# Performance work log

Hardware: AMD Instinct MI355X
Metric: run time of the kernel (lower is better)

Reference implementation:

```python
import jax, jax.numpy as jnp
import numpy as np

N_NODES = 100000
N_EDGES = 6400000
F_IN, F_HID, F_OUT = 5, 5, 10


def setup_inputs() -> dict:
    key = jax.random.key(0)
    ks = jax.random.split(key, 9)
    x = jax.random.normal(ks[0], (N_NODES, F_IN), dtype=jnp.float32)
    src = jax.random.randint(ks[1], (N_EDGES,), 0, N_NODES, dtype=jnp.int32)
    dst = jax.random.randint(ks[2], (N_EDGES,), 0, N_NODES, dtype=jnp.int32)
    s1 = 1.0 / np.sqrt(F_IN)
    s2 = 1.0 / np.sqrt(F_HID)
    W_self1 = jax.random.uniform(ks[3], (F_IN, F_HID), jnp.float32, -s1, s1)
    W_neigh1 = jax.random.uniform(ks[4], (F_IN, F_HID), jnp.float32, -s1, s1)
    b1 = jnp.zeros((F_HID,), jnp.float32)
    W_self2 = jax.random.uniform(ks[5], (F_HID, F_OUT), jnp.float32, -s2, s2)
    W_neigh2 = jax.random.uniform(ks[6], (F_HID, F_OUT), jnp.float32, -s2, s2)
    b2 = jnp.zeros((F_OUT,), jnp.float32)
    return {"x": x, "src": src, "dst": dst,
            "W_self1": W_self1, "W_neigh1": W_neigh1, "b1": b1,
            "W_self2": W_self2, "W_neigh2": W_neigh2, "b2": b2}


def _sage_mean(h, src, dst, W_self, W_neigh, b):
    # DGL SAGEConv (mean): out = h @ W_self + mean_{u->v}(h_u) @ W_neigh + b
    msg = h[src]                                        # [E, F] gather
    agg = jax.ops.segment_sum(msg, dst, num_segments=N_NODES)   # [N, F]
    deg = jax.ops.segment_sum(jnp.ones((src.shape[0],), h.dtype), dst,
                              num_segments=N_NODES)     # [N]
    h_neigh = agg / jnp.maximum(deg, 1.0)[:, None]
    return h @ W_self + h_neigh @ W_neigh + b


def reference(x, src, dst, W_self1, W_neigh1, b1, W_self2, W_neigh2, b2):
    h = jax.nn.sigmoid(_sage_mean(x, src, dst, W_self1, W_neigh1, b1))
    out = jax.nn.sigmoid(_sage_mean(h, src, dst, W_self2, W_neigh2, b2))
    return out
```

## Files before the change

### kernel.cpp

```cpp
#include <hip/hip_runtime.h>
#include <hip/hip_fp16.h>
#include <math.h>


#define F_IN  5
#define F_HID 5
#define F_OUT 10

#define NBSHIFT 7
#define NPB     (1 << NBSHIFT)
#define PBLK    1024
#define CHUNK   8192
#define EPT     8
#define BSTRIDE 9216
#define SBLK    512
#define SPT     18
#define LPN2    8
#define LBLK    256

__device__ __forceinline__ float sigmoidf(float v) {
    return 1.0f / (1.0f + __expf(-v));
}

__device__ __forceinline__ uint4 pack_h5(const float* __restrict__ xr) {
    float4 a = *(const float4*)xr;
    float a4 = xr[4];
    uint4 o;
    o.x = (unsigned)__half_as_ushort(__float2half_rn(a.x)) |
          ((unsigned)__half_as_ushort(__float2half_rn(a.y)) << 16);
    o.y = (unsigned)__half_as_ushort(__float2half_rn(a.z)) |
          ((unsigned)__half_as_ushort(__float2half_rn(a.w)) << 16);
    o.z = (unsigned)__half_as_ushort(__float2half_rn(a4));
    o.w = 0;
    return o;
}

__device__ __forceinline__ void acc5(uint4 q, float& a0, float& a1, float& a2,
                                     float& a3, float& a4) {
    float2 f01 = __half22float2(*(const __half2*)&q.x);
    float2 f23 = __half22float2(*(const __half2*)&q.y);
    float2 f45 = __half22float2(*(const __half2*)&q.z);
    a0 += f01.x; a1 += f01.y; a2 += f23.x; a3 += f23.y; a4 += f45.x;
}

__global__ void partition(const float* __restrict__ x,
                          const int* __restrict__ src, const int* __restrict__ dst,
                          int* __restrict__ bcursor, int* __restrict__ packed,
                          uint4* __restrict__ xh, int E, int N, int NB) {
    __shared__ int cnt[PBLK], excl[PBLK], adj[PBLK];
    __shared__ int wsum[16];
    __shared__ int buf[CHUNK];
    __shared__ unsigned char dlow[CHUNK];
    int t = threadIdx.x;
    int lane = t & 63, w = t >> 6;
    if (t < NPB) {
        int v = (blockIdx.x << NBSHIFT) + t;
        if (v < N) xh[v] = pack_h5(x + (size_t)v * 5);
    }
    cnt[t] = 0;
    __syncthreads();
    int base = blockIdx.x * CHUNK;
    int end  = min(base + CHUNK, E);
    int sarr[EPT], darr[EPT];
    #pragma unroll
    for (int r = 0; r < 2; ++r) {
        int i = base + r * 4096 + t * 4;
        if (i + 4 <= end) {
            int4 sv = *(const int4*)(src + i);
            int4 dv = *(const int4*)(dst + i);
            sarr[r*4+0]=sv.x; sarr[r*4+1]=sv.y; sarr[r*4+2]=sv.z; sarr[r*4+3]=sv.w;
            darr[r*4+0]=dv.x; darr[r*4+1]=dv.y; darr[r*4+2]=dv.z; darr[r*4+3]=dv.w;
        } else {
            #pragma unroll
            for (int c = 0; c < 4; ++c) {
                int i2 = i + c;
                if (i2 < end) { sarr[r*4+c] = src[i2]; darr[r*4+c] = dst[i2]; }
            }
        }
    }
    int esd[EPT];
    int ebp[EPT];
    #pragma unroll
    for (int j = 0; j < EPT; ++j) {
        int i = base + (j >> 2) * 4096 + t * 4 + (j & 3);
        if (i < end) {
            int sv = sarr[j], d = darr[j];
            int b  = d >> NBSHIFT;
            int p  = atomicAdd(&cnt[b], 1);
            esd[j] = sv | ((d & (NPB - 1)) << 17);
            ebp[j] = (b << 14) | p;
        }
    }
    __syncthreads();
    int v = cnt[t];
    int incl = v;
    #pragma unroll
    for (int off = 1; off < 64; off <<= 1) {
        int u = __shfl_up(incl, off, 64);
        if (lane >= off) incl += u;
    }
    if (lane == 63) wsum[w] = incl;
    __syncthreads();
    if (t < 16) {
        int s = wsum[t];
        #pragma unroll
        for (int off = 1; off < 16; off <<= 1) {
            int u = __shfl_up(s, off, 16);
            if (t >= off) s += u;
        }
        wsum[t] = s;
    }
    __syncthreads();
    int wbase = (w > 0) ? wsum[w - 1] : 0;
    excl[t] = incl - v + wbase;
    __syncthreads();
    if (t < NB) {
        int cb = cnt[t];
        int go = cb ? atomicAdd(&bcursor[t], cb) : 0;
        adj[t] = t * BSTRIDE + go - excl[t];
    }
    __syncthreads();
    #pragma unroll
    for (int j = 0; j < EPT; ++j) {
        int i = base + (j >> 2) * 4096 + t * 4 + (j & 3);
        if (i < end) {
            int b   = ebp[j] >> 14;
            int pos = excl[b] + (ebp[j] & 0x3FFF);
            buf[pos]  = (esd[j] & 0x1FFFF) | (b << 17);
            dlow[pos] = (unsigned char)(esd[j] >> 17);
        }
    }
    __syncthreads();
    int cval = end - base;
    for (int p = t; p < cval; p += PBLK) {
        int e = buf[p];
        int b = e >> 17;
        packed[adj[b] + p] = (e & 0x1FFFF) | ((int)dlow[p] << 17);
    }
}

__global__ void __launch_bounds__(SBLK, 8)
sortagg1(const uint4* __restrict__ xh, int* __restrict__ packed,
         const int* __restrict__ bcursor,
         const float* __restrict__ Ws, const float* __restrict__ Wn,
         const float* __restrict__ bias,
         uint4* __restrict__ hp, int2* __restrict__ sd, int N) {
    __shared__ int buf[BSTRIDE];
    __shared__ int ncnt[NPB], nst[NPB];
    __shared__ int w0sum;
    int b = blockIdx.x, t = threadIdx.x;
    int s0  = b * BSTRIDE;
    int cnt = min(bcursor[b], BSTRIDE);
    if (t < NPB) ncnt[t] = 0;
    __syncthreads();
    int myv[SPT];
    #pragma unroll
    for (int r = 0; r < 4; ++r) {
        int i = r * 2048 + t * 4;
        if (i + 4 <= cnt) {
            int4 q = *(const int4*)(packed + s0 + i);
            myv[r*4+0]=q.x; myv[r*4+1]=q.y; myv[r*4+2]=q.z; myv[r*4+3]=q.w;
        } else {
            #pragma unroll
            for (int c = 0; c < 4; ++c) {
                int i2 = i + c;
                myv[r*4+c] = (i2 < cnt) ? packed[s0 + i2] : 0;
            }
        }
    }
    {
        int i = 8192 + t * 2;
        if (i + 2 <= cnt) {
            int2 q = *(const int2*)(packed + s0 + i);
            myv[16] = q.x; myv[17] = q.y;
        } else {
            myv[16] = (i     < cnt) ? packed[s0 + i]     : 0;
            myv[17] = (i + 1 < cnt) ? packed[s0 + i + 1] : 0;
        }
    }
    short myp[SPT];
    #pragma unroll
    for (int j = 0; j < SPT; ++j) {
        int i = (j < 16) ? ((j >> 2) * 2048 + t * 4 + (j & 3)) : (8192 + t * 2 + (j - 16));
        if (i < cnt) {
            myp[j] = (short)atomicAdd(&ncnt[(myv[j] >> 17) & (NPB - 1)], 1);
        }
    }
    __syncthreads();
    if (t < NPB) {
        int lane = t & 63;
        int vv = ncnt[t];
        int incl = vv;
        #pragma unroll
        for (int off = 1; off < 64; off <<= 1) {
            int u = __shfl_up(incl, off, 64);
            if (lane >= off) incl += u;
        }
        if (t == 63) w0sum = incl;
        nst[t] = incl - vv;
    }
    __syncthreads();
    if (t >= 64 && t < NPB) nst[t] += w0sum;
    __syncthreads();
    if (t < NPB) {
        int node = (b << NBSHIFT) + t;
        if (node < N) sd[node] = make_int2(s0 + nst[t], ncnt[t]);
    }
    __syncthreads();
    #pragma unroll
    for (int j = 0; j < SPT; ++j) {
        int i = (j < 16) ? ((j >> 2) * 2048 + t * 4 + (j & 3)) : (8192 + t * 2 + (j - 16));
        if (i < cnt) {
            int e = myv[j];
            buf[nst[(e >> 17) & (NPB - 1)] + (int)myp[j]] = e;
        }
    }
    __syncthreads();
    for (int i = t * 4; i + 4 <= cnt; i += SBLK * 4) {
        int4 o = make_int4(buf[i] & 0x1FFFF, buf[i + 1] & 0x1FFFF,
                           buf[i + 2] & 0x1FFFF, buf[i + 3] & 0x1FFFF);
        *(int4*)(packed + s0 + i) = o;
    }
    {
        int tb = cnt & ~3;
        int i = tb + t;
        if (i < cnt) packed[s0 + i] = buf[i] & 0x1FFFF;
    }
    int sub = t & 3, ln = t >> 2;
    int node = (b << NBSHIFT) + ln;
    float a0 = 0, a1 = 0, a2 = 0, a3 = 0, a4 = 0;
    int dg = 0;
    if (node < N) {
        int st = nst[ln];
        dg = ncnt[ln];
        int k = sub;
        for (; k + 12 < dg; k += 16) {
            int u0 = buf[st + k]      & 0x1FFFF;
            int u1 = buf[st + k + 4]  & 0x1FFFF;
            int u2 = buf[st + k + 8]  & 0x1FFFF;
            int u3 = buf[st + k + 12] & 0x1FFFF;
            uint4 q0 = xh[u0];
            uint4 q1 = xh[u1];
            uint4 q2 = xh[u2];
            uint4 q3 = xh[u3];
            acc5(q0, a0, a1, a2, a3, a4);
            acc5(q1, a0, a1, a2, a3, a4);
            acc5(q2, a0, a1, a2, a3, a4);
            acc5(q3, a0, a1, a2, a3, a4);
        }
        for (; k < dg; k += 4) {
            int u = buf[st + k] & 0x1FFFF;
            acc5(xh[u], a0, a1, a2, a3, a4);
        }
    }
    #pragma unroll
    for (int off = 2; off > 0; off >>= 1) {
        a0 += __shfl_down(a0, off, 4);
        a1 += __shfl_down(a1, off, 4);
        a2 += __shfl_down(a2, off, 4);
        a3 += __shfl_down(a3, off, 4);
        a4 += __shfl_down(a4, off, 4);
    }
    if (sub != 0 || node >= N) return;
    float rd = 1.0f / fmaxf((float)dg, 1.0f);
    float ni[F_IN] = { a0 * rd, a1 * rd, a2 * rd, a3 * rd, a4 * rd };
    uint4 qs = xh[node];
    float2 s01 = __half22float2(*(const __half2*)&qs.x);
    float2 s23 = __half22float2(*(const __half2*)&qs.y);
    float2 s45 = __half22float2(*(const __half2*)&qs.z);
    float xi[F_IN] = { s01.x, s01.y, s23.x, s23.y, s45.x };
    unsigned short hu[5];
    #pragma unroll
    for (int j = 0; j < F_HID; ++j) {
        float acc = bias[j];
        #pragma unroll
        for (int f = 0; f < F_IN; ++f)
            acc += xi[f] * Ws[f * F_HID + j] + ni[f] * Wn[f * F_HID + j];
        hu[j] = __half_as_ushort(__float2half_rn(sigmoidf(acc)));
    }
    uint4 o;
    o.x = (unsigned)hu[0] | ((unsigned)hu[1] << 16);
    o.y = (unsigned)hu[2] | ((unsigned)hu[3] << 16);
    o.z = (unsigned)hu[4];
    o.w = 0;
    hp[node] = o;
}

__global__ void layer2(const uint4* __restrict__ hp, const int* __restrict__ eidx,
                       const int2* __restrict__ sd,
                       const float* __restrict__ Ws, const float* __restrict__ Wn,
                       const float* __restrict__ b,
                       float* __restrict__ out, int N) {
    int tid = blockIdx.x * blockDim.x + threadIdx.x;
    int v   = tid >> 3;
    int sub = threadIdx.x & (LPN2 - 1);
    if (v >= N) return;
    int2 sdv = sd[v];
    int st = sdv.x, dg = sdv.y;
    int len = (dg + LPN2 - 1) >> 3;
    int k0 = sub * len;
    int k1 = min(k0 + len, dg);
    float s0 = 0, s1 = 0, s2 = 0, s3 = 0, s4 = 0;
    int k = k0;
    for (; k + 4 <= k1; k += 4) {
        int4 qi;
        __builtin_memcpy(&qi, eidx + st + k, 16);
        uint4 q0 = hp[qi.x];
        uint4 q1 = hp[qi.y];
        uint4 q2 = hp[qi.z];
        uint4 q3 = hp[qi.w];
        acc5(q0, s0, s1, s2, s3, s4);
        acc5(q1, s0, s1, s2, s3, s4);
        acc5(q2, s0, s1, s2, s3, s4);
        acc5(q3, s0, s1, s2, s3, s4);
    }
    for (; k < k1; ++k) {
        int u = eidx[st + k];
        acc5(hp[u], s0, s1, s2, s3, s4);
    }
    #pragma unroll
    for (int off = LPN2 / 2; off > 0; off >>= 1) {
        s0 += __shfl_down(s0, off, LPN2);
        s1 += __shfl_down(s1, off, LPN2);
        s2 += __shfl_down(s2, off, LPN2);
        s3 += __shfl_down(s3, off, LPN2);
        s4 += __shfl_down(s4, off, LPN2);
    }
    if (sub != 0) return;
    float rd = 1.0f / fmaxf((float)dg, 1.0f);
    float ni[F_HID] = { s0 * rd, s1 * rd, s2 * rd, s3 * rd, s4 * rd };
    uint4 q = hp[v];
    float2 f01 = __half22float2(*(const __half2*)&q.x);
    float2 f23 = __half22float2(*(const __half2*)&q.y);
    float2 f45 = __half22float2(*(const __half2*)&q.z);
    float hi[F_HID] = { f01.x, f01.y, f23.x, f23.y, f45.x };
    #pragma unroll
    for (int j = 0; j < F_OUT; ++j) {
        float acc = b[j];
        #pragma unroll
        for (int f = 0; f < F_HID; ++f)
            acc += hi[f] * Ws[f * F_OUT + j] + ni[f] * Wn[f * F_OUT + j];
        out[(size_t)v * F_OUT + j] = sigmoidf(acc);
    }
}

extern "C" void kernel_launch(void* const* d_in, const int* in_sizes, int n_in,
                              void* d_out, int out_size, void* d_ws, size_t ws_size,
                              hipStream_t stream) {
    const float* x   = (const float*)d_in[0];
    const int*   src = (const int*)d_in[1];
    const int*   dst = (const int*)d_in[2];
    const float* Ws1 = (const float*)d_in[3];
    const float* Wn1 = (const float*)d_in[4];
    const float* b1  = (const float*)d_in[5];
    const float* Ws2 = (const float*)d_in[6];
    const float* Wn2 = (const float*)d_in[7];
    const float* b2  = (const float*)d_in[8];
    float* out = (float*)d_out;

    const int N  = in_sizes[0] / F_IN;
    const int E  = in_sizes[1];
    const int NB = (N + NPB - 1) >> NBSHIFT;

    int*   bcursor = (int*)d_ws;
    uint4* xh      = (uint4*)(bcursor + 1024);
    int2*  sd      = (int2*)(xh + N);
    int*   packed  = (int*)(sd + N);
    uint4* hp      = (uint4*)(packed + (size_t)NB * BSTRIDE);

    const int ablocks = (E + CHUNK - 1) / CHUNK;
    const int lgrid   = ((size_t)N * LPN2 + LBLK - 1) / LBLK;

    (void)hipMemsetAsync(bcursor, 0, 1024 * sizeof(int), stream);
    partition<<<ablocks, PBLK, 0, stream>>>(x, src, dst, bcursor, packed, xh, E, N, NB);
    sortagg1<<<NB, SBLK, 0, stream>>>(xh, packed, bcursor, Ws1, Wn1, b1, hp, sd, N);
    layer2<<<lgrid, LBLK, 0, stream>>>(hp, packed, sd, Ws2, Wn2, b2, out, N);
}
```

Baseline: 201.9 us.

## Halve node bucket size to 64 nodes, doubling sort blocks

Node buckets shrink from 128 to 64 nodes, so there are about 1563 buckets instead of 782. The partition kernel now handles up to 2048 bucket counters, with each thread scanning two buckets, and it reuses the counter array to hold the write offsets. The per-bucket sort kernel uses 256 threads and a half-size shared buffer, so more blocks fit per CU and the grid is larger. The single-wave scan removes two barriers. In exchange, partition does more scattered global writes into smaller bucket segments, and its shared-memory use grows.

```diff
diff --git a/kernel.cpp b/kernel.cpp
--- a/kernel.cpp
+++ b/kernel.cpp
@@ -7,13 +7,13 @@
 #define F_HID 5
 #define F_OUT 10
 
-#define NBSHIFT 7
+#define NBSHIFT 6
 #define NPB     (1 << NBSHIFT)
 #define PBLK    1024
 #define CHUNK   8192
 #define EPT     8
-#define BSTRIDE 9216
-#define SBLK    512
+#define BSTRIDE 4608
+#define SBLK    256
 #define SPT     18
 #define LPN2    8
 #define LBLK    256
@@ -47,17 +47,19 @@
                           const int* __restrict__ src, const int* __restrict__ dst,
                           int* __restrict__ bcursor, int* __restrict__ packed,
                           uint4* __restrict__ xh, int E, int N, int NB) {
-    __shared__ int cnt[PBLK], excl[PBLK], adj[PBLK];
+    __shared__ int cnt[2048];
+    __shared__ int excl[2048];
     __shared__ int wsum[16];
     __shared__ int buf[CHUNK];
     __shared__ unsigned char dlow[CHUNK];
     int t = threadIdx.x;
     int lane = t & 63, w = t >> 6;
-    if (t < NPB) {
-        int v = (blockIdx.x << NBSHIFT) + t;
+    if (t < 128) {
+        int v = blockIdx.x * 128 + t;
         if (v < N) xh[v] = pack_h5(x + (size_t)v * 5);
     }
     cnt[t] = 0;
+    cnt[t + 1024] = 0;
     __syncthreads();
     int base = blockIdx.x * CHUNK;
     int end  = min(base + CHUNK, E);
@@ -92,8 +94,10 @@
         }
     }
     __syncthreads();
-    int v = cnt[t];
-    int incl = v;
+    int c0 = (2 * t     < NB) ? cnt[2 * t]     : 0;
+    int c1 = (2 * t + 1 < NB) ? cnt[2 * t + 1] : 0;
+    int s = c0 + c1;
+    int incl = s;
     #pragma unroll
     for (int off = 1; off < 64; off <<= 1) {
         int u = __shfl_up(incl, off, 64);
@@ -102,22 +106,24 @@
     if (lane == 63) wsum[w] = incl;
     __syncthreads();
     if (t < 16) {
-        int s = wsum[t];
+        int sv = wsum[t];
         #pragma unroll
         for (int off = 1; off < 16; off <<= 1) {
-            int u = __shfl_up(s, off, 16);
-            if (t >= off) s += u;
-        }
-        wsum[t] = s;
+            int u = __shfl_up(sv, off, 16);
+            if (t >= off) sv += u;
+        }
+        wsum[t] = sv;
     }
     __syncthreads();
     int wbase = (w > 0) ? wsum[w - 1] : 0;
-    excl[t] = incl - v + wbase;
-    __syncthreads();
-    if (t < NB) {
-        int cb = cnt[t];
-        int go = cb ? atomicAdd(&bcursor[t], cb) : 0;
-        adj[t] = t * BSTRIDE + go - excl[t];
+    int e0 = incl - s + wbase;
+    if (2 * t     < NB) excl[2 * t]     = e0;
+    if (2 * t + 1 < NB) excl[2 * t + 1] = e0 + c0;
+    __syncthreads();
+    for (int bb = t; bb < NB; bb += PBLK) {
+        int cb = cnt[bb];
+        int go = cb ? atomicAdd(&bcursor[bb], cb) : 0;
+        cnt[bb] = bb * BSTRIDE + go - excl[bb];
     }
     __syncthreads();
     #pragma unroll
@@ -135,7 +141,7 @@
     for (int p = t; p < cval; p += PBLK) {
         int e = buf[p];
         int b = e >> 17;
-        packed[adj[b] + p] = (e & 0x1FFFF) | ((int)dlow[p] << 17);
+        packed[cnt[b] + p] = (e & 0x1FFFF) | ((int)dlow[p] << 17);
     }
 }
 
@@ -147,7 +153,6 @@
          uint4* __restrict__ hp, int2* __restrict__ sd, int N) {
     __shared__ int buf[BSTRIDE];
     __shared__ int ncnt[NPB], nst[NPB];
-    __shared__ int w0sum;
     int b = blockIdx.x, t = threadIdx.x;
     int s0  = b * BSTRIDE;
     int cnt = min(bcursor[b], BSTRIDE);
@@ -156,7 +161,7 @@
     int myv[SPT];
     #pragma unroll
     for (int r = 0; r < 4; ++r) {
-        int i = r * 2048 + t * 4;
+        int i = r * 1024 + t * 4;
         if (i + 4 <= cnt) {
             int4 q = *(const int4*)(packed + s0 + i);
             myv[r*4+0]=q.x; myv[r*4+1]=q.y; myv[r*4+2]=q.z; myv[r*4+3]=q.w;
@@ -169,7 +174,7 @@
         }
     }
     {
-        int i = 8192 + t * 2;
+        int i = 4096 + t * 2;
         if (i + 2 <= cnt) {
             int2 q = *(const int2*)(packed + s0 + i);
             myv[16] = q.x; myv[17] = q.y;
@@ -181,35 +186,28 @@
     short myp[SPT];
     #pragma unroll
     for (int j = 0; j < SPT; ++j) {
-        int i = (j < 16) ? ((j >> 2) * 2048 + t * 4 + (j & 3)) : (8192 + t * 2 + (j - 16));
+        int i = (j < 16) ? ((j >> 2) * 1024 + t * 4 + (j & 3)) : (4096 + t * 2 + (j - 16));
         if (i < cnt) {
             myp[j] = (short)atomicAdd(&ncnt[(myv[j] >> 17) & (NPB - 1)], 1);
         }
     }
     __syncthreads();
     if (t < NPB) {
-        int lane = t & 63;
         int vv = ncnt[t];
         int incl = vv;
         #pragma unroll
         for (int off = 1; off < 64; off <<= 1) {
             int u = __shfl_up(incl, off, 64);
-            if (lane >= off) incl += u;
-        }
-        if (t == 63) w0sum = incl;
+            if (t >= off) incl += u;
+        }
         nst[t] = incl - vv;
-    }
-    __syncthreads();
-    if (t >= 64 && t < NPB) nst[t] += w0sum;
-    __syncthreads();
-    if (t < NPB) {
         int node = (b << NBSHIFT) + t;
-        if (node < N) sd[node] = make_int2(s0 + nst[t], ncnt[t]);
+        if (node < N) sd[node] = make_int2(s0 + incl - vv, vv);
     }
     __syncthreads();
     #pragma unroll
     for (int j = 0; j < SPT; ++j) {
-        int i = (j < 16) ? ((j >> 2) * 2048 + t * 4 + (j & 3)) : (8192 + t * 2 + (j - 16));
+        int i = (j < 16) ? ((j >> 2) * 1024 + t * 4 + (j & 3)) : (4096 + t * 2 + (j - 16));
         if (i < cnt) {
             int e = myv[j];
             buf[nst[(e >> 17) & (NPB - 1)] + (int)myp[j]] = e;
@@ -363,7 +361,7 @@
     const int NB = (N + NPB - 1) >> NBSHIFT;
 
     int*   bcursor = (int*)d_ws;
-    uint4* xh      = (uint4*)(bcursor + 1024);
+    uint4* xh      = (uint4*)(bcursor + 2048);
     int2*  sd      = (int2*)(xh + N);
     int*   packed  = (int*)(sd + N);
     uint4* hp      = (uint4*)(packed + (size_t)NB * BSTRIDE);
@@ -371,7 +369,7 @@
     const int ablocks = (E + CHUNK - 1) / CHUNK;
     const int lgrid   = ((size_t)N * LPN2 + LBLK - 1) / LBLK;
 
-    (void)hipMemsetAsync(bcursor, 0, 1024 * sizeof(int), stream);
+    (void)hipMemsetAsync(bcursor, 0, 2048 * sizeof(int), stream);
     partition<<<ablocks, PBLK, 0, stream>>>(x, src, dst, bcursor, packed, xh, E, N, NB);
     sortagg1<<<NB, SBLK, 0, stream>>>(xh, packed, bcursor, Ws1, Wn1, b1, hp, sd, N);
     layer2<<<lgrid, LBLK, 0, stream>>>(hp, packed, sd, Ws2, Wn2, b2, out, N);
```

After: 207.6 us. 2.8% more time.

## Redo per-bucket sort in layer 2 instead of writing sorted edges back

Applied to the files above, without the earlier changes.

Layer 1 no longer writes the sorted source indices and per-node offsets back to global memory. Layer 2 becomes a bucket kernel that reloads the partitioned edges, re-sorts them in shared memory by destination, and aggregates. This drops a global write of all edges plus the offset array, at the cost of repeating the shared-memory counting sort and using one block per bucket instead of a fine-grained grid. Output stores are also vectorised to float2.

```diff
diff --git a/kernel.cpp b/kernel.cpp
--- a/kernel.cpp
+++ b/kernel.cpp
@@ -15,8 +15,6 @@
 #define BSTRIDE 9216
 #define SBLK    512
 #define SPT     18
-#define LPN2    8
-#define LBLK    256
 
 __device__ __forceinline__ float sigmoidf(float v) {
     return 1.0f / (1.0f + __expf(-v));
@@ -140,11 +138,11 @@
 }
 
 __global__ void __launch_bounds__(SBLK, 8)
-sortagg1(const uint4* __restrict__ xh, int* __restrict__ packed,
+sortagg1(const uint4* __restrict__ xh, const int* __restrict__ packed,
          const int* __restrict__ bcursor,
          const float* __restrict__ Ws, const float* __restrict__ Wn,
          const float* __restrict__ bias,
-         uint4* __restrict__ hp, int2* __restrict__ sd, int N) {
+         uint4* __restrict__ hp, int N) {
     __shared__ int buf[BSTRIDE];
     __shared__ int ncnt[NPB], nst[NPB];
     __shared__ int w0sum;
@@ -202,11 +200,6 @@
     __syncthreads();
     if (t >= 64 && t < NPB) nst[t] += w0sum;
     __syncthreads();
-    if (t < NPB) {
-        int node = (b << NBSHIFT) + t;
-        if (node < N) sd[node] = make_int2(s0 + nst[t], ncnt[t]);
-    }
-    __syncthreads();
     #pragma unroll
     for (int j = 0; j < SPT; ++j) {
         int i = (j < 16) ? ((j >> 2) * 2048 + t * 4 + (j & 3)) : (8192 + t * 2 + (j - 16));
@@ -216,16 +209,6 @@
         }
     }
     __syncthreads();
-    for (int i = t * 4; i + 4 <= cnt; i += SBLK * 4) {
-        int4 o = make_int4(buf[i] & 0x1FFFF, buf[i + 1] & 0x1FFFF,
-                           buf[i + 2] & 0x1FFFF, buf[i + 3] & 0x1FFFF);
-        *(int4*)(packed + s0 + i) = o;
-    }
-    {
-        int tb = cnt & ~3;
-        int i = tb + t;
-        if (i < cnt) packed[s0 + i] = buf[i] & 0x1FFFF;
-    }
     int sub = t & 3, ln = t >> 2;
     int node = (b << NBSHIFT) + ln;
     float a0 = 0, a1 = 0, a2 = 0, a3 = 0, a4 = 0;
@@ -286,62 +269,134 @@
     hp[node] = o;
 }
 
-__global__ void layer2(const uint4* __restrict__ hp, const int* __restrict__ eidx,
-                       const int2* __restrict__ sd,
-                       const float* __restrict__ Ws, const float* __restrict__ Wn,
-                       const float* __restrict__ b,
-                       float* __restrict__ out, int N) {
-    int tid = blockIdx.x * blockDim.x + threadIdx.x;
-    int v   = tid >> 3;
-    int sub = threadIdx.x & (LPN2 - 1);
-    if (v >= N) return;
-    int2 sdv = sd[v];
-    int st = sdv.x, dg = sdv.y;
-    int len = (dg + LPN2 - 1) >> 3;
-    int k0 = sub * len;
-    int k1 = min(k0 + len, dg);
-    float s0 = 0, s1 = 0, s2 = 0, s3 = 0, s4 = 0;
-    int k = k0;
-    for (; k + 4 <= k1; k += 4) {
-        int4 qi;
-        __builtin_memcpy(&qi, eidx + st + k, 16);
-        uint4 q0 = hp[qi.x];
-        uint4 q1 = hp[qi.y];
-        uint4 q2 = hp[qi.z];
-        uint4 q3 = hp[qi.w];
-        acc5(q0, s0, s1, s2, s3, s4);
-        acc5(q1, s0, s1, s2, s3, s4);
-        acc5(q2, s0, s1, s2, s3, s4);
-        acc5(q3, s0, s1, s2, s3, s4);
-    }
-    for (; k < k1; ++k) {
-        int u = eidx[st + k];
-        acc5(hp[u], s0, s1, s2, s3, s4);
-    }
-    #pragma unroll
-    for (int off = LPN2 / 2; off > 0; off >>= 1) {
-        s0 += __shfl_down(s0, off, LPN2);
-        s1 += __shfl_down(s1, off, LPN2);
-        s2 += __shfl_down(s2, off, LPN2);
-        s3 += __shfl_down(s3, off, LPN2);
-        s4 += __shfl_down(s4, off, LPN2);
-    }
-    if (sub != 0) return;
+__global__ void __launch_bounds__(SBLK, 8)
+sortagg2(const uint4* __restrict__ hp, const int* __restrict__ packed,
+         const int* __restrict__ bcursor,
+         const float* __restrict__ Ws, const float* __restrict__ Wn,
+         const float* __restrict__ bias,
+         float* __restrict__ out, int N) {
+    __shared__ int buf[BSTRIDE];
+    __shared__ int ncnt[NPB], nst[NPB];
+    __shared__ int w0sum;
+    int b = blockIdx.x, t = threadIdx.x;
+    int s0  = b * BSTRIDE;
+    int cnt = min(bcursor[b], BSTRIDE);
+    if (t < NPB) ncnt[t] = 0;
+    __syncthreads();
+    int myv[SPT];
+    #pragma unroll
+    for (int r = 0; r < 4; ++r) {
+        int i = r * 2048 + t * 4;
+        if (i + 4 <= cnt) {
+            int4 q = *(const int4*)(packed + s0 + i);
+            myv[r*4+0]=q.x; myv[r*4+1]=q.y; myv[r*4+2]=q.z; myv[r*4+3]=q.w;
+        } else {
+            #pragma unroll
+            for (int c = 0; c < 4; ++c) {
+                int i2 = i + c;
+                myv[r*4+c] = (i2 < cnt) ? packed[s0 + i2] : 0;
+            }
+        }
+    }
+    {
+        int i = 8192 + t * 2;
+        if (i + 2 <= cnt) {
+            int2 q = *(const int2*)(packed + s0 + i);
+            myv[16] = q.x; myv[17] = q.y;
+        } else {
+            myv[16] = (i     < cnt) ? packed[s0 + i]     : 0;
+            myv[17] = (i + 1 < cnt) ? packed[s0 + i + 1] : 0;
+        }
+    }
+    short myp[SPT];
+    #pragma unroll
+    for (int j = 0; j < SPT; ++j) {
+        int i = (j < 16) ? ((j >> 2) * 2048 + t * 4 + (j & 3)) : (8192 + t * 2 + (j - 16));
+        if (i < cnt) {
+            myp[j] = (short)atomicAdd(&ncnt[(myv[j] >> 17) & (NPB - 1)], 1);
+        }
+    }
+    __syncthreads();
+    if (t < NPB) {
+        int lane = t & 63;
+        int vv = ncnt[t];
+        int incl = vv;
+        #pragma unroll
+        for (int off = 1; off < 64; off <<= 1) {
+            int u = __shfl_up(incl, off, 64);
+            if (lane >= off) incl += u;
+        }
+        if (t == 63) w0sum = incl;
+        nst[t] = incl - vv;
+    }
+    __syncthreads();
+    if (t >= 64 && t < NPB) nst[t] += w0sum;
+    __syncthreads();
+    #pragma unroll
+    for (int j = 0; j < SPT; ++j) {
+        int i = (j < 16) ? ((j >> 2) * 2048 + t * 4 + (j & 3)) : (8192 + t * 2 + (j - 16));
+        if (i < cnt) {
+            int e = myv[j];
+            buf[nst[(e >> 17) & (NPB - 1)] + (int)myp[j]] = e;
+        }
+    }
+    __syncthreads();
+    int sub = t & 3, ln = t >> 2;
+    int node = (b << NBSHIFT) + ln;
+    float a0 = 0, a1 = 0, a2 = 0, a3 = 0, a4 = 0;
+    int dg = 0;
+    if (node < N) {
+        int st = nst[ln];
+        dg = ncnt[ln];
+        int k = sub;
+        for (; k + 12 < dg; k += 16) {
+            int u0 = buf[st + k]      & 0x1FFFF;
+            int u1 = buf[st + k + 4]  & 0x1FFFF;
+            int u2 = buf[st + k + 8]  & 0x1FFFF;
+            int u3 = buf[st + k + 12] & 0x1FFFF;
+            uint4 q0 = hp[u0];
+            uint4 q1 = hp[u1];
+            uint4 q2 = hp[u2];
+            uint4 q3 = hp[u3];
+            acc5(q0, a0, a1, a2, a3, a4);
+            acc5(q1, a0, a1, a2, a3, a4);
+            acc5(q2, a0, a1, a2, a3, a4);
+            acc5(q3, a0, a1, a2, a3, a4);
+        }
+        for (; k < dg; k += 4) {
+            int u = buf[st + k] & 0x1FFFF;
+            acc5(hp[u], a0, a1, a2, a3, a4);
+        }
+    }
+    #pragma unroll
+    for (int off = 2; off > 0; off >>= 1) {
+        a0 += __shfl_down(a0, off, 4);
+        a1 += __shfl_down(a1, off, 4);
+        a2 += __shfl_down(a2, off, 4);
+        a3 += __shfl_down(a3, off, 4);
+        a4 += __shfl_down(a4, off, 4);
+    }
+    if (sub != 0 || node >= N) return;
     float rd = 1.0f / fmaxf((float)dg, 1.0f);
-    float ni[F_HID] = { s0 * rd, s1 * rd, s2 * rd, s3 * rd, s4 * rd };
-    uint4 q = hp[v];
+    float ni[F_HID] = { a0 * rd, a1 * rd, a2 * rd, a3 * rd, a4 * rd };
+    uint4 q = hp[node];
     float2 f01 = __half22float2(*(const __half2*)&q.x);
     float2 f23 = __half22float2(*(const __half2*)&q.y);
     float2 f45 = __half22float2(*(const __half2*)&q.z);
     float hi[F_HID] = { f01.x, f01.y, f23.x, f23.y, f45.x };
+    float o[F_OUT];
     #pragma unroll
     for (int j = 0; j < F_OUT; ++j) {
-        float acc = b[j];
+        float acc = bias[j];
         #pragma unroll
         for (int f = 0; f < F_HID; ++f)
             acc += hi[f] * Ws[f * F_OUT + j] + ni[f] * Wn[f * F_OUT + j];
-        out[(size_t)v * F_OUT + j] = sigmoidf(acc);
-    }
+        o[j] = sigmoidf(acc);
+    }
+    float* op = out + (size_t)node * F_OUT;
+    #pragma unroll
+    for (int j = 0; j < F_OUT; j += 2)
+        *(float2*)(op + j) = make_float2(o[j], o[j + 1]);
 }
 
 extern "C" void kernel_launch(void* const* d_in, const int* in_sizes, int n_in,
@@ -364,15 +419,13 @@
 
     int*   bcursor = (int*)d_ws;
     uint4* xh      = (uint4*)(bcursor + 1024);
-    int2*  sd      = (int2*)(xh + N);
-    int*   packed  = (int*)(sd + N);
+    int*   packed  = (int*)(xh + N);
     uint4* hp      = (uint4*)(packed + (size_t)NB * BSTRIDE);
 
     const int ablocks = (E + CHUNK - 1) / CHUNK;
-    const int lgrid   = ((size_t)N * LPN2 + LBLK - 1) / LBLK;
 
     (void)hipMemsetAsync(bcursor, 0, 1024 * sizeof(int), stream);
     partition<<<ablocks, PBLK, 0, stream>>>(x, src, dst, bcursor, packed, xh, E, N, NB);
-    sortagg1<<<NB, SBLK, 0, stream>>>(xh, packed, bcursor, Ws1, Wn1, b1, hp, sd, N);
-    layer2<<<lgrid, LBLK, 0, stream>>>(hp, packed, sd, Ws2, Wn2, b2, out, N);
-}
+    sortagg1<<<NB, SBLK, 0, stream>>>(xh, packed, bcursor, Ws1, Wn1, b1, hp, N);
+    sortagg2<<<NB, SBLK, 0, stream>>>(hp, packed, bcursor, Ws2, Wn2, b2, out, N);
+}
```

Result: no change. 202.6 us (+0.4%).
